# Kernel tuning notes

Measured on AMD Instinct MI355X. Metric: run time of the kernel, lower is better.

## Reference

```python
import jax, jax.numpy as jnp
import numpy as np

D_MODEL = 768
NUM_HEADS = 12
HEAD_DIM = D_MODEL // NUM_HEADS
LN_EPS = 1e-5
MASK_NEG = -1000000.0


def setup_inputs() -> dict:
    key = jax.random.key(0)
    ks = jax.random.split(key, 10)
    B, L, S = 2, 2048, 2048
    s = 1.0 / np.sqrt(D_MODEL)
    return {
        "q": jax.random.normal(ks[0], (B, L, D_MODEL), jnp.float32),
        "k": jax.random.normal(ks[1], (B, S, D_MODEL), jnp.float32),
        "v": jax.random.normal(ks[2], (B, S, D_MODEL), jnp.float32),
        "attention_mask": jnp.ones((B, S), jnp.int32),
        "Wq": jax.random.normal(ks[3], (D_MODEL, D_MODEL), jnp.float32) * s,
        "Wk": jax.random.normal(ks[4], (D_MODEL, D_MODEL), jnp.float32) * s,
        "Wv": jax.random.normal(ks[5], (D_MODEL, D_MODEL), jnp.float32) * s,
        "W": jax.random.normal(ks[6], (D_MODEL, D_MODEL), jnp.float32) * s,
        "b": jnp.zeros((D_MODEL,), jnp.float32),
        "gamma": jnp.ones((D_MODEL,), jnp.float32),
        "beta": jnp.zeros((D_MODEL,), jnp.float32),
    }


def reference(q, k, v, attention_mask, Wq, Wk, Wv, W, b, gamma, beta):
    B, L, D = q.shape
    S = k.shape[1]
    H, hd = NUM_HEADS, HEAD_DIM
    # projections (torch Linear: x @ W^T), split heads -> (B,H,L,hd)
    Q = (q @ Wq.T).reshape(B, L, H, hd).transpose(0, 2, 1, 3)
    K = (k @ Wk.T).reshape(B, S, H, hd).transpose(0, 2, 1, 3)
    V = (v @ Wv.T).reshape(B, S, H, hd).transpose(0, 2, 1, 3)
    # scores (B,H,L,S) with additive key-padding mask
    scores = jnp.einsum("bhld,bhsd->bhls", Q, K) / np.sqrt(hd)
    mask_score = (1.0 - attention_mask.astype(q.dtype))[:, None, None, :] * MASK_NEG
    att = jax.nn.softmax(scores + mask_score, axis=-1)  # dropout p=0 (eval)
    # attend, merge heads, output projection (with bias)
    O = jnp.einsum("bhls,bhsd->bhld", att, V).transpose(0, 2, 1, 3).reshape(B, L, D)
    O = O @ W.T + b  # state dropout p=0 (eval)
    # residual + LayerNorm
    x = q + O
    mu = jnp.mean(x, axis=-1, keepdims=True)
    var = jnp.mean(jnp.square(x - mu), axis=-1, keepdims=True)
    return (x - mu) * jax.lax.rsqrt(var + LN_EPS) * gamma + beta
```

## Files before the change

### kernel.cpp

```cpp
#include <hip/hip_runtime.h>
#include <hip/hip_bf16.h>
#include <math.h>


typedef unsigned short u16;
typedef unsigned int   u32;
typedef __bf16 bf16x8 __attribute__((ext_vector_type(8)));
typedef float  f32x4  __attribute__((ext_vector_type(4)));

#define DM   768
#define MR   4096
#define WSZ  589824

#define LOG2E 1.44269504089f
#define SM_C  15.0f
#define K1    (0.125f * LOG2E)

__device__ inline u16 bfbits(float f) {
    union { __bf16 b; u16 u; } x; x.b = (__bf16)f; return x.u;
}

__device__ inline uint4 cvt8(const float* src) {
    const float4* p = reinterpret_cast<const float4*>(src);
    float4 a = p[0], b = p[1];
    union { __bf16 h[8]; uint4 v; } u;
    u.h[0] = (__bf16)a.x; u.h[1] = (__bf16)a.y; u.h[2] = (__bf16)a.z; u.h[3] = (__bf16)a.w;
    u.h[4] = (__bf16)b.x; u.h[5] = (__bf16)b.y; u.h[6] = (__bf16)b.z; u.h[7] = (__bf16)b.w;
    return u.v;
}

__global__ __launch_bounds__(256) void wcvt(
    const float* __restrict__ w0, const float* __restrict__ w1,
    const float* __restrict__ w2, const float* __restrict__ w3,
    u16* __restrict__ dst)
{
    const float* src = (blockIdx.y == 0) ? w0 : (blockIdx.y == 1) ? w1
                     : (blockIdx.y == 2) ? w2 : w3;
    size_t idx = ((size_t)blockIdx.x * 256 + threadIdx.x) * 8;
    *reinterpret_cast<uint4*>(&dst[(size_t)blockIdx.y * WSZ + idx]) = cvt8(&src[idx]);
}

__global__ __launch_bounds__(256) void gemm_qkv(
    const float* __restrict__ xq, const float* __restrict__ xk, const float* __restrict__ xv,
    const u16* __restrict__ Wb4,
    u16* __restrict__ oq, u16* __restrict__ ok, u16* __restrict__ ov)
{
    const int mode = blockIdx.z;
    const float* X = (mode == 0) ? xq : (mode == 1) ? xk : xv;
    const u16* Wb  = Wb4 + (size_t)mode * WSZ;
    u16* out       = (mode == 0) ? oq : (mode == 1) ? ok : ov;

    __shared__ __attribute__((aligned(16))) u16 As[64][72];
    __shared__ __attribute__((aligned(16))) u16 Bs[64][72];

    const int tid  = threadIdx.x;
    const int lane = tid & 63;
    const int w    = tid >> 6;
    const int wm   = (w >> 1) * 32;
    const int wn   = (w & 1) * 32;
    const int quad = lane >> 4;
    const int l16  = lane & 15;
    const int tm   = blockIdx.x * 64;
    const int tn   = blockIdx.y * 64;

    f32x4 acc[2][2] = {};

    for (int k0 = 0; k0 < 768; k0 += 64) {
        __syncthreads();
        #pragma unroll
        for (int rep = 0; rep < 2; rep++) {
            int idx = tid + rep * 256;
            int row = idx >> 3;
            int col = (idx & 7) * 8;
            *reinterpret_cast<uint4*>(&As[row][col]) = cvt8(&X[(size_t)(tm + row) * 768 + k0 + col]);
            *reinterpret_cast<uint4*>(&Bs[row][col]) =
                *reinterpret_cast<const uint4*>(&Wb[(size_t)(tn + row) * 768 + k0 + col]);
        }
        __syncthreads();
        #pragma unroll
        for (int kk = 0; kk < 2; kk++) {
            bf16x8 a0 = *reinterpret_cast<const bf16x8*>(&As[wm + l16     ][kk*32 + quad*8]);
            bf16x8 a1 = *reinterpret_cast<const bf16x8*>(&As[wm + 16 + l16][kk*32 + quad*8]);
            bf16x8 b0 = *reinterpret_cast<const bf16x8*>(&Bs[wn + l16     ][kk*32 + quad*8]);
            bf16x8 b1 = *reinterpret_cast<const bf16x8*>(&Bs[wn + 16 + l16][kk*32 + quad*8]);
            acc[0][0] = __builtin_amdgcn_mfma_f32_16x16x32_bf16(a0, b0, acc[0][0], 0, 0, 0);
            acc[0][1] = __builtin_amdgcn_mfma_f32_16x16x32_bf16(a0, b1, acc[0][1], 0, 0, 0);
            acc[1][0] = __builtin_amdgcn_mfma_f32_16x16x32_bf16(a1, b0, acc[1][0], 0, 0, 0);
            acc[1][1] = __builtin_amdgcn_mfma_f32_16x16x32_bf16(a1, b1, acc[1][1], 0, 0, 0);
        }
    }

    #pragma unroll
    for (int i = 0; i < 2; i++)
        #pragma unroll
        for (int j = 0; j < 2; j++)
            #pragma unroll
            for (int r = 0; r < 4; r++) {
                int gm = tm + wm + i * 16 + quad * 4 + r;
                int gn = tn + wn + j * 16 + l16;
                int b = gm >> 11, l = gm & 2047;
                int h = gn >> 6,  d = gn & 63;
                u16 bv = bfbits(acc[i][j][r]);
                if (mode == 2)
                    out[((size_t)(b * 12 + h) * 64 + d) * 2048 + l] = bv;
                else
                    out[((size_t)(b * 12 + h) * 2048 + l) * 64 + d] = bv;
            }
}

__global__ __launch_bounds__(256) void gemm_out(
    const u16* __restrict__ Oa, const u16* __restrict__ Wb,
    const float* __restrict__ bias, const float* __restrict__ resid,
    float* __restrict__ Xb)
{
    __shared__ __attribute__((aligned(16))) u16 As[64][72];
    __shared__ __attribute__((aligned(16))) u16 Bs[64][72];

    const int tid  = threadIdx.x;
    const int lane = tid & 63;
    const int w    = tid >> 6;
    const int wm   = (w >> 1) * 32;
    const int wn   = (w & 1) * 32;
    const int quad = lane >> 4;
    const int l16  = lane & 15;
    const int tm   = blockIdx.x * 64;
    const int tn   = blockIdx.y * 64;

    f32x4 acc[2][2] = {};

    for (int k0 = 0; k0 < 768; k0 += 64) {
        __syncthreads();
        #pragma unroll
        for (int rep = 0; rep < 2; rep++) {
            int idx = tid + rep * 256;
            int row = idx >> 3;
            int col = (idx & 7) * 8;
            *reinterpret_cast<uint4*>(&As[row][col]) =
                *reinterpret_cast<const uint4*>(&Oa[(size_t)(tm + row) * 768 + k0 + col]);
            *reinterpret_cast<uint4*>(&Bs[row][col]) =
                *reinterpret_cast<const uint4*>(&Wb[(size_t)(tn + row) * 768 + k0 + col]);
        }
        __syncthreads();
        #pragma unroll
        for (int kk = 0; kk < 2; kk++) {
            bf16x8 a0 = *reinterpret_cast<const bf16x8*>(&As[wm + l16     ][kk*32 + quad*8]);
            bf16x8 a1 = *reinterpret_cast<const bf16x8*>(&As[wm + 16 + l16][kk*32 + quad*8]);
            bf16x8 b0 = *reinterpret_cast<const bf16x8*>(&Bs[wn + l16     ][kk*32 + quad*8]);
            bf16x8 b1 = *reinterpret_cast<const bf16x8*>(&Bs[wn + 16 + l16][kk*32 + quad*8]);
            acc[0][0] = __builtin_amdgcn_mfma_f32_16x16x32_bf16(a0, b0, acc[0][0], 0, 0, 0);
            acc[0][1] = __builtin_amdgcn_mfma_f32_16x16x32_bf16(a0, b1, acc[0][1], 0, 0, 0);
            acc[1][0] = __builtin_amdgcn_mfma_f32_16x16x32_bf16(a1, b0, acc[1][0], 0, 0, 0);
            acc[1][1] = __builtin_amdgcn_mfma_f32_16x16x32_bf16(a1, b1, acc[1][1], 0, 0, 0);
        }
    }

    #pragma unroll
    for (int i = 0; i < 2; i++)
        #pragma unroll
        for (int j = 0; j < 2; j++)
            #pragma unroll
            for (int r = 0; r < 4; r++) {
                int gm = tm + wm + i * 16 + quad * 4 + r;
                int gn = tn + wn + j * 16 + l16;
                Xb[(size_t)gm * 768 + gn] = acc[i][j][r] + bias[gn] + resid[(size_t)gm * 768 + gn];
            }
}

__global__ __launch_bounds__(256, 3) void attn(
    const u16* __restrict__ Qp, const u16* __restrict__ Kp, const u16* __restrict__ Vt,
    const int* __restrict__ amask, u16* __restrict__ Oatt)
{
    __shared__ __attribute__((aligned(16))) unsigned char smem[4 * 64 * 40 * 2 + 2048 * 4];
    u16 (*Ps)[64][40] = reinterpret_cast<u16(*)[64][40]>(smem);
    float* maskC = reinterpret_cast<float*>(smem + 20480);
    float (*Obuf)[72] = reinterpret_cast<float(*)[72]>(smem);

    const int tid  = threadIdx.x;
    const int lane = tid & 63;
    const int w    = tid >> 6;
    const int quad = lane >> 4;
    const int l16  = lane & 15;
    const int qt = blockIdx.x;
    const int h  = blockIdx.y;
    const int b  = blockIdx.z;

    #pragma unroll
    for (int i = 0; i < 8; i++) {
        int s = tid + i * 256;
        maskC[s] = amask[b * 2048 + s] ? (-SM_C * LOG2E) : -2.0e6f;
    }
    __syncthreads();

    const u16* Qbase = Qp + ((size_t)(b * 12 + h) * 2048 + qt * 64) * 64;
    const u16* Kb2   = Kp + (size_t)(b * 12 + h) * 2048 * 64 + (size_t)w * 32 * 64;
    const u16* Vb2   = Vt + (size_t)(b * 12 + h) * 64 * 2048 + (size_t)w * 32;

    bf16x8 qfrag[4][2];
    #pragma unroll
    for (int qb = 0; qb < 4; qb++)
        #pragma unroll
        for (int kk = 0; kk < 2; kk++)
            qfrag[qb][kk] = *reinterpret_cast<const bf16x8*>(
                &Qbase[(qb * 16 + l16) * 64 + kk * 32 + quad * 8]);

    bf16x8 onesf = {};
    if (l16 == 0) {
        #pragma unroll
        for (int i = 0; i < 8; i++) onesf[i] = (__bf16)1.0f;
    }

    f32x4 oacc[4][4] = {};
    f32x4 sacc[4]    = {};

    for (int st = 0; st < 16; st++) {
        bf16x8 kf[2][2], vf[4];
        #pragma unroll
        for (int ct = 0; ct < 2; ct++)
            #pragma unroll
            for (int kk = 0; kk < 2; kk++)
                kf[ct][kk] = *reinterpret_cast<const bf16x8*>(
                    &Kb2[(size_t)(st * 128 + ct * 16 + l16) * 64 + kk * 32 + quad * 8]);
        #pragma unroll
        for (int cd = 0; cd < 4; cd++)
            vf[cd] = *reinterpret_cast<const bf16x8*>(
                &Vb2[(size_t)(cd * 16 + l16) * 2048 + st * 128 + quad * 8]);

        float cc0 = maskC[st * 128 + w * 32 + l16];
        float cc1 = maskC[st * 128 + w * 32 + 16 + l16];

        #pragma unroll
        for (int qb = 0; qb < 4; qb++)
            #pragma unroll
            for (int ct = 0; ct < 2; ct++) {
                f32x4 s = {};
                s = __builtin_amdgcn_mfma_f32_16x16x32_bf16(qfrag[qb][0], kf[ct][0], s, 0, 0, 0);
                s = __builtin_amdgcn_mfma_f32_16x16x32_bf16(qfrag[qb][1], kf[ct][1], s, 0, 0, 0);
                float cc = ct ? cc1 : cc0;
                #pragma unroll
                for (int r = 0; r < 4; r++) {
                    float p = __builtin_amdgcn_exp2f(__builtin_fmaf(s[r], K1, cc));
                    Ps[w][qb * 16 + quad * 4 + r][ct * 16 + l16] = bfbits(p);
                }
            }

        bf16x8 pf[4];
        #pragma unroll
        for (int qb = 0; qb < 4; qb++)
            pf[qb] = *reinterpret_cast<const bf16x8*>(&Ps[w][qb * 16 + l16][quad * 8]);
        #pragma unroll
        for (int qb = 0; qb < 4; qb++)
            sacc[qb] = __builtin_amdgcn_mfma_f32_16x16x32_bf16(pf[qb], onesf, sacc[qb], 0, 0, 0);
        #pragma unroll
        for (int qb = 0; qb < 4; qb++)
            #pragma unroll
            for (int cd = 0; cd < 4; cd++)
                oacc[qb][cd] = __builtin_amdgcn_mfma_f32_16x16x32_bf16(pf[qb], vf[cd], oacc[qb][cd], 0, 0, 0);
    }

    __syncthreads();
    for (int wv = 0; wv < 4; wv++) {
        if (w == wv) {
            #pragma unroll
            for (int qb = 0; qb < 4; qb++) {
                #pragma unroll
                for (int cd = 0; cd < 4; cd++)
                    #pragma unroll
                    for (int r = 0; r < 4; r++) {
                        float* cell = &Obuf[qb * 16 + quad * 4 + r][cd * 16 + l16];
                        if (wv == 0) *cell = oacc[qb][cd][r];
                        else         *cell += oacc[qb][cd][r];
                    }
                if (l16 == 0) {
                    #pragma unroll
                    for (int r = 0; r < 4; r++) {
                        float* cell = &Obuf[qb * 16 + quad * 4 + r][64];
                        if (wv == 0) *cell = sacc[qb][r];
                        else         *cell += sacc[qb][r];
                    }
                }
            }
        }
        __syncthreads();
    }

    #pragma unroll
    for (int g = 0; g < 4; g++) {
        int unit = tid + g * 256;
        int row = unit >> 4;
        int c4  = (unit & 15) * 4;
        float rinv = 1.0f / Obuf[row][64];
        union { u16 h[4]; uint2 v; } o;
        #pragma unroll
        for (int j = 0; j < 4; j++)
            o.h[j] = bfbits(Obuf[row][c4 + j] * rinv);
        *reinterpret_cast<uint2*>(
            &Oatt[(size_t)(b * 2048 + qt * 64 + row) * 768 + h * 64 + c4]) = o.v;
    }
}

__global__ __launch_bounds__(256) void ln_kernel(
    float* __restrict__ X, const float* __restrict__ gamma,
    const float* __restrict__ beta)
{
    const int row = blockIdx.x;
    const int tid = threadIdx.x;
    float* xr = X + (size_t)row * 768;

    float v[3], s = 0.f, s2 = 0.f;
    #pragma unroll
    for (int i = 0; i < 3; i++) {
        v[i] = xr[tid + i * 256];
        s += v[i];
        s2 += v[i] * v[i];
    }
    #pragma unroll
    for (int off = 32; off >= 1; off >>= 1) {
        s  += __shfl_xor(s,  off, 64);
        s2 += __shfl_xor(s2, off, 64);
    }
    __shared__ float rs[4], rs2[4];
    int w = tid >> 6, lane = tid & 63;
    if (lane == 0) { rs[w] = s; rs2[w] = s2; }
    __syncthreads();
    s  = rs[0] + rs[1] + rs[2] + rs[3];
    s2 = rs2[0] + rs2[1] + rs2[2] + rs2[3];
    float mu = s * (1.0f / 768.0f);
    float var = s2 * (1.0f / 768.0f) - mu * mu;
    float rstd = rsqrtf(var + 1e-5f);
    #pragma unroll
    for (int i = 0; i < 3; i++) {
        int c = tid + i * 256;
        xr[c] = (v[i] - mu) * rstd * gamma[c] + beta[c];
    }
}

extern "C" void kernel_launch(void* const* d_in, const int* in_sizes, int n_in,
                              void* d_out, int out_size, void* d_ws, size_t ws_size,
                              hipStream_t stream)
{
    const float* q   = (const float*)d_in[0];
    const float* k   = (const float*)d_in[1];
    const float* v   = (const float*)d_in[2];
    const int*   am  = (const int*)d_in[3];
    const float* Wq  = (const float*)d_in[4];
    const float* Wk  = (const float*)d_in[5];
    const float* Wv  = (const float*)d_in[6];
    const float* W   = (const float*)d_in[7];
    const float* bb  = (const float*)d_in[8];
    const float* gam = (const float*)d_in[9];
    const float* bet = (const float*)d_in[10];

    u16* Wb4 = (u16*)d_ws;
    u16* Qp  = Wb4 + (size_t)4 * WSZ;
    u16* Kp  = Qp + (size_t)MR * DM;
    u16* Vt  = Kp + (size_t)MR * DM;
    u16* Oa  = Vt + (size_t)MR * DM;
    float* Xb = (float*)d_out;

    wcvt<<<dim3(288, 4), 256, 0, stream>>>(Wq, Wk, Wv, W, Wb4);
    gemm_qkv<<<dim3(64, 12, 3), 256, 0, stream>>>(q, k, v, Wb4, Qp, Kp, Vt);
    attn<<<dim3(32, 12, 2), 256, 0, stream>>>(Qp, Kp, Vt, am, Oa);
    gemm_out<<<dim3(64, 12), 256, 0, stream>>>(Oa, Wb4 + (size_t)3 * WSZ, bb, q, Xb);
    ln_kernel<<<4096, 256, 0, stream>>>(Xb, gam, bet);
}
```

Baseline: 226.3 us.

## Enlarge QKV GEMM tiles to 128x128 with double-buffered register prefetch

The QKV projection GEMM moves from 64x64 to 128x128 block tiles, with each wave computing a 64x64 sub-tile of 4x4 MFMAs. Shared memory is double-buffered, and the next K-slice is loaded into registers while the current one is computed, so each iteration needs only one barrier. This raises data reuse per global load and hides load latency. In exchange it uses more registers and LDS, and the grid shrinks to 576 blocks, which may leave some CUs underused.

```diff
diff --git a/kernel.cpp b/kernel.cpp
--- a/kernel.cpp
+++ b/kernel.cpp
@@ -29,6 +29,13 @@
     return u.v;
 }
 
+__device__ inline uint4 cvt8v(float4 a, float4 b) {
+    union { __bf16 h[8]; uint4 v; } u;
+    u.h[0] = (__bf16)a.x; u.h[1] = (__bf16)a.y; u.h[2] = (__bf16)a.z; u.h[3] = (__bf16)a.w;
+    u.h[4] = (__bf16)b.x; u.h[5] = (__bf16)b.y; u.h[6] = (__bf16)b.z; u.h[7] = (__bf16)b.w;
+    return u.v;
+}
+
 __global__ __launch_bounds__(256) void wcvt(
     const float* __restrict__ w0, const float* __restrict__ w1,
     const float* __restrict__ w2, const float* __restrict__ w3,
@@ -40,7 +47,7 @@
     *reinterpret_cast<uint4*>(&dst[(size_t)blockIdx.y * WSZ + idx]) = cvt8(&src[idx]);
 }
 
-__global__ __launch_bounds__(256) void gemm_qkv(
+__global__ __launch_bounds__(256, 2) void gemm_qkv(
     const float* __restrict__ xq, const float* __restrict__ xk, const float* __restrict__ xv,
     const u16* __restrict__ Wb4,
     u16* __restrict__ oq, u16* __restrict__ ok, u16* __restrict__ ov)
@@ -50,50 +57,88 @@
     const u16* Wb  = Wb4 + (size_t)mode * WSZ;
     u16* out       = (mode == 0) ? oq : (mode == 1) ? ok : ov;
 
-    __shared__ __attribute__((aligned(16))) u16 As[64][72];
-    __shared__ __attribute__((aligned(16))) u16 Bs[64][72];
+    __shared__ __attribute__((aligned(16))) u16 As[2][128][72];
+    __shared__ __attribute__((aligned(16))) u16 Bs[2][128][72];
 
     const int tid  = threadIdx.x;
     const int lane = tid & 63;
     const int w    = tid >> 6;
-    const int wm   = (w >> 1) * 32;
-    const int wn   = (w & 1) * 32;
+    const int wm   = (w >> 1) * 64;
+    const int wn   = (w & 1) * 64;
     const int quad = lane >> 4;
     const int l16  = lane & 15;
-    const int tm   = blockIdx.x * 64;
-    const int tn   = blockIdx.y * 64;
-
-    f32x4 acc[2][2] = {};
-
-    for (int k0 = 0; k0 < 768; k0 += 64) {
+    const int tm   = blockIdx.x * 128;
+    const int tn   = blockIdx.y * 128;
+
+    const int srow = tid >> 1;
+    const int scb  = (tid & 1) * 32;
+
+    const float* aptr = &X[(size_t)(tm + srow) * 768 + scb];
+    const u16*   bptr = &Wb[(size_t)(tn + srow) * 768 + scb];
+
+    f32x4 acc[4][4] = {};
+
+    {
+        float4 at[8]; uint4 bt[4];
+        #pragma unroll
+        for (int i = 0; i < 8; i++)
+            at[i] = *reinterpret_cast<const float4*>(aptr + i * 4);
+        #pragma unroll
+        for (int i = 0; i < 4; i++)
+            bt[i] = *reinterpret_cast<const uint4*>(bptr + i * 8);
+        #pragma unroll
+        for (int i = 0; i < 4; i++) {
+            *reinterpret_cast<uint4*>(&As[0][srow][scb + i * 8]) = cvt8v(at[2*i], at[2*i+1]);
+            *reinterpret_cast<uint4*>(&Bs[0][srow][scb + i * 8]) = bt[i];
+        }
+    }
+
+    for (int kt = 0; kt < 12; kt++) {
+        const int cur = kt & 1;
         __syncthreads();
-        #pragma unroll
-        for (int rep = 0; rep < 2; rep++) {
-            int idx = tid + rep * 256;
-            int row = idx >> 3;
-            int col = (idx & 7) * 8;
-            *reinterpret_cast<uint4*>(&As[row][col]) = cvt8(&X[(size_t)(tm + row) * 768 + k0 + col]);
-            *reinterpret_cast<uint4*>(&Bs[row][col]) =
-                *reinterpret_cast<const uint4*>(&Wb[(size_t)(tn + row) * 768 + k0 + col]);
-        }
-        __syncthreads();
+
+        float4 at[8]; uint4 bt[4];
+        if (kt < 11) {
+            const float* ap = aptr + (kt + 1) * 64;
+            const u16*   bp = bptr + (kt + 1) * 64;
+            #pragma unroll
+            for (int i = 0; i < 8; i++)
+                at[i] = *reinterpret_cast<const float4*>(ap + i * 4);
+            #pragma unroll
+            for (int i = 0; i < 4; i++)
+                bt[i] = *reinterpret_cast<const uint4*>(bp + i * 8);
+        }
+
         #pragma unroll
         for (int kk = 0; kk < 2; kk++) {
-            bf16x8 a0 = *reinterpret_cast<const bf16x8*>(&As[wm + l16     ][kk*32 + quad*8]);
-            bf16x8 a1 = *reinterpret_cast<const bf16x8*>(&As[wm + 16 + l16][kk*32 + quad*8]);
-            bf16x8 b0 = *reinterpret_cast<const bf16x8*>(&Bs[wn + l16     ][kk*32 + quad*8]);
-            bf16x8 b1 = *reinterpret_cast<const bf16x8*>(&Bs[wn + 16 + l16][kk*32 + quad*8]);
-            acc[0][0] = __builtin_amdgcn_mfma_f32_16x16x32_bf16(a0, b0, acc[0][0], 0, 0, 0);
-            acc[0][1] = __builtin_amdgcn_mfma_f32_16x16x32_bf16(a0, b1, acc[0][1], 0, 0, 0);
-            acc[1][0] = __builtin_amdgcn_mfma_f32_16x16x32_bf16(a1, b0, acc[1][0], 0, 0, 0);
-            acc[1][1] = __builtin_amdgcn_mfma_f32_16x16x32_bf16(a1, b1, acc[1][1], 0, 0, 0);
-        }
-    }
-
-    #pragma unroll
-    for (int i = 0; i < 2; i++)
-        #pragma unroll
-        for (int j = 0; j < 2; j++)
+            bf16x8 af[4], bfr[4];
+            #pragma unroll
+            for (int i = 0; i < 4; i++)
+                af[i] = *reinterpret_cast<const bf16x8*>(&As[cur][wm + i * 16 + l16][kk * 32 + quad * 8]);
+            #pragma unroll
+            for (int j = 0; j < 4; j++)
+                bfr[j] = *reinterpret_cast<const bf16x8*>(&Bs[cur][wn + j * 16 + l16][kk * 32 + quad * 8]);
+            #pragma unroll
+            for (int i = 0; i < 4; i++)
+                #pragma unroll
+                for (int j = 0; j < 4; j++)
+                    acc[i][j] = __builtin_amdgcn_mfma_f32_16x16x32_bf16(af[i], bfr[j], acc[i][j], 0, 0, 0);
+        }
+
+        if (kt < 11) {
+            const int nxt = cur ^ 1;
+            #pragma unroll
+            for (int i = 0; i < 4; i++) {
+                *reinterpret_cast<uint4*>(&As[nxt][srow][scb + i * 8]) = cvt8v(at[2*i], at[2*i+1]);
+                *reinterpret_cast<uint4*>(&Bs[nxt][srow][scb + i * 8]) = bt[i];
+            }
+        }
+    }
+
+    #pragma unroll
+    for (int i = 0; i < 4; i++)
+        #pragma unroll
+        for (int j = 0; j < 4; j++)
             #pragma unroll
             for (int r = 0; r < 4; r++) {
                 int gm = tm + wm + i * 16 + quad * 4 + r;
@@ -358,7 +403,7 @@
     float* Xb = (float*)d_out;
 
     wcvt<<<dim3(288, 4), 256, 0, stream>>>(Wq, Wk, Wv, W, Wb4);
-    gemm_qkv<<<dim3(64, 12, 3), 256, 0, stream>>>(q, k, v, Wb4, Qp, Kp, Vt);
+    gemm_qkv<<<dim3(32, 6, 3), 256, 0, stream>>>(q, k, v, Wb4, Qp, Kp, Vt);
     attn<<<dim3(32, 12, 2), 256, 0, stream>>>(Qp, Kp, Vt, am, Oa);
     gemm_out<<<dim3(64, 12), 256, 0, stream>>>(Oa, Wb4 + (size_t)3 * WSZ, bb, q, Xb);
     ln_kernel<<<4096, 256, 0, stream>>>(Xb, gam, bet);
```

Result: slower. 247.4 us (+9.3%).

## Double-buffer GEMM shared tiles and transpose score MFMA for packed P stores

Applied to the files above, without the earlier changes.

Both projection GEMMs now use two shared-memory buffers and register prefetch of the next K tile, so global loads overlap with the MFMAs and one barrier per iteration is removed. Launch bounds request two blocks per CU. In attention, the score MFMA operands are swapped so each lane holds four consecutive key columns. This lets the mask load as one f32x4 and the P tile be written as a single 8-byte packed store instead of four scattered 2-byte stores. Shared-memory use doubles in the GEMMs, which could lower occupancy.

```diff
diff --git a/kernel.cpp b/kernel.cpp
--- a/kernel.cpp
+++ b/kernel.cpp
@@ -29,6 +29,13 @@
     return u.v;
 }
 
+__device__ inline uint4 cvt8v(float4 a, float4 b) {
+    union { __bf16 h[8]; uint4 v; } u;
+    u.h[0] = (__bf16)a.x; u.h[1] = (__bf16)a.y; u.h[2] = (__bf16)a.z; u.h[3] = (__bf16)a.w;
+    u.h[4] = (__bf16)b.x; u.h[5] = (__bf16)b.y; u.h[6] = (__bf16)b.z; u.h[7] = (__bf16)b.w;
+    return u.v;
+}
+
 __global__ __launch_bounds__(256) void wcvt(
     const float* __restrict__ w0, const float* __restrict__ w1,
     const float* __restrict__ w2, const float* __restrict__ w3,
@@ -40,7 +47,7 @@
     *reinterpret_cast<uint4*>(&dst[(size_t)blockIdx.y * WSZ + idx]) = cvt8(&src[idx]);
 }
 
-__global__ __launch_bounds__(256) void gemm_qkv(
+__global__ __launch_bounds__(256, 2) void gemm_qkv(
     const float* __restrict__ xq, const float* __restrict__ xk, const float* __restrict__ xv,
     const u16* __restrict__ Wb4,
     u16* __restrict__ oq, u16* __restrict__ ok, u16* __restrict__ ov)
@@ -50,8 +57,8 @@
     const u16* Wb  = Wb4 + (size_t)mode * WSZ;
     u16* out       = (mode == 0) ? oq : (mode == 1) ? ok : ov;
 
-    __shared__ __attribute__((aligned(16))) u16 As[64][72];
-    __shared__ __attribute__((aligned(16))) u16 Bs[64][72];
+    __shared__ __attribute__((aligned(16))) u16 As[2][64][72];
+    __shared__ __attribute__((aligned(16))) u16 Bs[2][64][72];
 
     const int tid  = threadIdx.x;
     const int lane = tid & 63;
@@ -63,30 +70,56 @@
     const int tm   = blockIdx.x * 64;
     const int tn   = blockIdx.y * 64;
 
+    const int row0 = tid >> 3,         col0 = (tid & 7) * 8;
+    const int row1 = (tid + 256) >> 3, col1 = ((tid + 256) & 7) * 8;
+
+    const float* a0p = &X[(size_t)(tm + row0) * 768 + col0];
+    const float* a1p = &X[(size_t)(tm + row1) * 768 + col1];
+    const u16*   b0p = &Wb[(size_t)(tn + row0) * 768 + col0];
+    const u16*   b1p = &Wb[(size_t)(tn + row1) * 768 + col1];
+
     f32x4 acc[2][2] = {};
 
-    for (int k0 = 0; k0 < 768; k0 += 64) {
+    {
+        *reinterpret_cast<uint4*>(&As[0][row0][col0]) = cvt8(a0p);
+        *reinterpret_cast<uint4*>(&As[0][row1][col1]) = cvt8(a1p);
+        *reinterpret_cast<uint4*>(&Bs[0][row0][col0]) = *reinterpret_cast<const uint4*>(b0p);
+        *reinterpret_cast<uint4*>(&Bs[0][row1][col1]) = *reinterpret_cast<const uint4*>(b1p);
+    }
+
+    for (int kt = 0; kt < 12; kt++) {
+        const int cur = kt & 1;
         __syncthreads();
-        #pragma unroll
-        for (int rep = 0; rep < 2; rep++) {
-            int idx = tid + rep * 256;
-            int row = idx >> 3;
-            int col = (idx & 7) * 8;
-            *reinterpret_cast<uint4*>(&As[row][col]) = cvt8(&X[(size_t)(tm + row) * 768 + k0 + col]);
-            *reinterpret_cast<uint4*>(&Bs[row][col]) =
-                *reinterpret_cast<const uint4*>(&Wb[(size_t)(tn + row) * 768 + k0 + col]);
-        }
-        __syncthreads();
+
+        float4 af0a, af0b, af1a, af1b; uint4 bt0, bt1;
+        if (kt < 11) {
+            const int ko = (kt + 1) * 64;
+            af0a = *reinterpret_cast<const float4*>(a0p + ko);
+            af0b = *reinterpret_cast<const float4*>(a0p + ko + 4);
+            af1a = *reinterpret_cast<const float4*>(a1p + ko);
+            af1b = *reinterpret_cast<const float4*>(a1p + ko + 4);
+            bt0  = *reinterpret_cast<const uint4*>(b0p + ko);
+            bt1  = *reinterpret_cast<const uint4*>(b1p + ko);
+        }
+
         #pragma unroll
         for (int kk = 0; kk < 2; kk++) {
-            bf16x8 a0 = *reinterpret_cast<const bf16x8*>(&As[wm + l16     ][kk*32 + quad*8]);
-            bf16x8 a1 = *reinterpret_cast<const bf16x8*>(&As[wm + 16 + l16][kk*32 + quad*8]);
-            bf16x8 b0 = *reinterpret_cast<const bf16x8*>(&Bs[wn + l16     ][kk*32 + quad*8]);
-            bf16x8 b1 = *reinterpret_cast<const bf16x8*>(&Bs[wn + 16 + l16][kk*32 + quad*8]);
+            bf16x8 a0 = *reinterpret_cast<const bf16x8*>(&As[cur][wm + l16     ][kk*32 + quad*8]);
+            bf16x8 a1 = *reinterpret_cast<const bf16x8*>(&As[cur][wm + 16 + l16][kk*32 + quad*8]);
+            bf16x8 b0 = *reinterpret_cast<const bf16x8*>(&Bs[cur][wn + l16     ][kk*32 + quad*8]);
+            bf16x8 b1 = *reinterpret_cast<const bf16x8*>(&Bs[cur][wn + 16 + l16][kk*32 + quad*8]);
             acc[0][0] = __builtin_amdgcn_mfma_f32_16x16x32_bf16(a0, b0, acc[0][0], 0, 0, 0);
             acc[0][1] = __builtin_amdgcn_mfma_f32_16x16x32_bf16(a0, b1, acc[0][1], 0, 0, 0);
             acc[1][0] = __builtin_amdgcn_mfma_f32_16x16x32_bf16(a1, b0, acc[1][0], 0, 0, 0);
             acc[1][1] = __builtin_amdgcn_mfma_f32_16x16x32_bf16(a1, b1, acc[1][1], 0, 0, 0);
+        }
+
+        if (kt < 11) {
+            const int nxt = cur ^ 1;
+            *reinterpret_cast<uint4*>(&As[nxt][row0][col0]) = cvt8v(af0a, af0b);
+            *reinterpret_cast<uint4*>(&As[nxt][row1][col1]) = cvt8v(af1a, af1b);
+            *reinterpret_cast<uint4*>(&Bs[nxt][row0][col0]) = bt0;
+            *reinterpret_cast<uint4*>(&Bs[nxt][row1][col1]) = bt1;
         }
     }
 
@@ -108,13 +141,13 @@
             }
 }
 
-__global__ __launch_bounds__(256) void gemm_out(
+__global__ __launch_bounds__(256, 2) void gemm_out(
     const u16* __restrict__ Oa, const u16* __restrict__ Wb,
     const float* __restrict__ bias, const float* __restrict__ resid,
     float* __restrict__ Xb)
 {
-    __shared__ __attribute__((aligned(16))) u16 As[64][72];
-    __shared__ __attribute__((aligned(16))) u16 Bs[64][72];
+    __shared__ __attribute__((aligned(16))) u16 As[2][64][72];
+    __shared__ __attribute__((aligned(16))) u16 Bs[2][64][72];
 
     const int tid  = threadIdx.x;
     const int lane = tid & 63;
@@ -126,31 +159,54 @@
     const int tm   = blockIdx.x * 64;
     const int tn   = blockIdx.y * 64;
 
+    const int row0 = tid >> 3,         col0 = (tid & 7) * 8;
+    const int row1 = (tid + 256) >> 3, col1 = ((tid + 256) & 7) * 8;
+
+    const u16* a0p = &Oa[(size_t)(tm + row0) * 768 + col0];
+    const u16* a1p = &Oa[(size_t)(tm + row1) * 768 + col1];
+    const u16* b0p = &Wb[(size_t)(tn + row0) * 768 + col0];
+    const u16* b1p = &Wb[(size_t)(tn + row1) * 768 + col1];
+
     f32x4 acc[2][2] = {};
 
-    for (int k0 = 0; k0 < 768; k0 += 64) {
+    {
+        *reinterpret_cast<uint4*>(&As[0][row0][col0]) = *reinterpret_cast<const uint4*>(a0p);
+        *reinterpret_cast<uint4*>(&As[0][row1][col1]) = *reinterpret_cast<const uint4*>(a1p);
+        *reinterpret_cast<uint4*>(&Bs[0][row0][col0]) = *reinterpret_cast<const uint4*>(b0p);
+        *reinterpret_cast<uint4*>(&Bs[0][row1][col1]) = *reinterpret_cast<const uint4*>(b1p);
+    }
+
+    for (int kt = 0; kt < 12; kt++) {
+        const int cur = kt & 1;
         __syncthreads();
-        #pragma unroll
-        for (int rep = 0; rep < 2; rep++) {
-            int idx = tid + rep * 256;
-            int row = idx >> 3;
-            int col = (idx & 7) * 8;
-            *reinterpret_cast<uint4*>(&As[row][col]) =
-                *reinterpret_cast<const uint4*>(&Oa[(size_t)(tm + row) * 768 + k0 + col]);
-            *reinterpret_cast<uint4*>(&Bs[row][col]) =
-                *reinterpret_cast<const uint4*>(&Wb[(size_t)(tn + row) * 768 + k0 + col]);
-        }
-        __syncthreads();
+
+        uint4 at0, at1, bt0, bt1;
+        if (kt < 11) {
+            const int ko = (kt + 1) * 64;
+            at0 = *reinterpret_cast<const uint4*>(a0p + ko);
+            at1 = *reinterpret_cast<const uint4*>(a1p + ko);
+            bt0 = *reinterpret_cast<const uint4*>(b0p + ko);
+            bt1 = *reinterpret_cast<const uint4*>(b1p + ko);
+        }
+
         #pragma unroll
         for (int kk = 0; kk < 2; kk++) {
-            bf16x8 a0 = *reinterpret_cast<const bf16x8*>(&As[wm + l16     ][kk*32 + quad*8]);
-            bf16x8 a1 = *reinterpret_cast<const bf16x8*>(&As[wm + 16 + l16][kk*32 + quad*8]);
-            bf16x8 b0 = *reinterpret_cast<const bf16x8*>(&Bs[wn + l16     ][kk*32 + quad*8]);
-            bf16x8 b1 = *reinterpret_cast<const bf16x8*>(&Bs[wn + 16 + l16][kk*32 + quad*8]);
+            bf16x8 a0 = *reinterpret_cast<const bf16x8*>(&As[cur][wm + l16     ][kk*32 + quad*8]);
+            bf16x8 a1 = *reinterpret_cast<const bf16x8*>(&As[cur][wm + 16 + l16][kk*32 + quad*8]);
+            bf16x8 b0 = *reinterpret_cast<const bf16x8*>(&Bs[cur][wn + l16     ][kk*32 + quad*8]);
+            bf16x8 b1 = *reinterpret_cast<const bf16x8*>(&Bs[cur][wn + 16 + l16][kk*32 + quad*8]);
             acc[0][0] = __builtin_amdgcn_mfma_f32_16x16x32_bf16(a0, b0, acc[0][0], 0, 0, 0);
             acc[0][1] = __builtin_amdgcn_mfma_f32_16x16x32_bf16(a0, b1, acc[0][1], 0, 0, 0);
             acc[1][0] = __builtin_amdgcn_mfma_f32_16x16x32_bf16(a1, b0, acc[1][0], 0, 0, 0);
             acc[1][1] = __builtin_amdgcn_mfma_f32_16x16x32_bf16(a1, b1, acc[1][1], 0, 0, 0);
+        }
+
+        if (kt < 11) {
+            const int nxt = cur ^ 1;
+            *reinterpret_cast<uint4*>(&As[nxt][row0][col0]) = at0;
+            *reinterpret_cast<uint4*>(&As[nxt][row1][col1]) = at1;
+            *reinterpret_cast<uint4*>(&Bs[nxt][row0][col0]) = bt0;
+            *reinterpret_cast<uint4*>(&Bs[nxt][row1][col1]) = bt1;
         }
     }
 
@@ -225,22 +281,20 @@
             vf[cd] = *reinterpret_cast<const bf16x8*>(
                 &Vb2[(size_t)(cd * 16 + l16) * 2048 + st * 128 + quad * 8]);
 
-        float cc0 = maskC[st * 128 + w * 32 + l16];
-        float cc1 = maskC[st * 128 + w * 32 + 16 + l16];
-
         #pragma unroll
         for (int qb = 0; qb < 4; qb++)
             #pragma unroll
             for (int ct = 0; ct < 2; ct++) {
                 f32x4 s = {};
-                s = __builtin_amdgcn_mfma_f32_16x16x32_bf16(qfrag[qb][0], kf[ct][0], s, 0, 0, 0);
-                s = __builtin_amdgcn_mfma_f32_16x16x32_bf16(qfrag[qb][1], kf[ct][1], s, 0, 0, 0);
-                float cc = ct ? cc1 : cc0;
+                s = __builtin_amdgcn_mfma_f32_16x16x32_bf16(kf[ct][0], qfrag[qb][0], s, 0, 0, 0);
+                s = __builtin_amdgcn_mfma_f32_16x16x32_bf16(kf[ct][1], qfrag[qb][1], s, 0, 0, 0);
+                f32x4 cc = *reinterpret_cast<const f32x4*>(
+                    &maskC[st * 128 + w * 32 + ct * 16 + quad * 4]);
+                union { u16 h[4]; uint2 v2; } pk;
                 #pragma unroll
-                for (int r = 0; r < 4; r++) {
-                    float p = __builtin_amdgcn_exp2f(__builtin_fmaf(s[r], K1, cc));
-                    Ps[w][qb * 16 + quad * 4 + r][ct * 16 + l16] = bfbits(p);
-                }
+                for (int r = 0; r < 4; r++)
+                    pk.h[r] = bfbits(__builtin_amdgcn_exp2f(__builtin_fmaf(s[r], K1, cc[r])));
+                *reinterpret_cast<uint2*>(&Ps[w][qb * 16 + l16][ct * 16 + quad * 4]) = pk.v2;
             }
 
         bf16x8 pf[4];
```

After: 217.3 us. 1.04x faster.
